# Optimization experiments

Measured on AMD Instinct MI355X. Metric: run time of the kernel, lower is better.

## Reference

```python
import jax, jax.numpy as jnp
import numpy as np

# Grid / model constants (from cfg: scene_bbox [0,0,0,102.4,102.4,6.4], featmap_size=quant_size=0.4, n_input=5, batch=2)
B, N = 2, 300000
X, Y, Z, T = 256, 256, 16, 5
QUANT = np.array([0.4, 0.4, 0.4, 1.0], dtype=np.float32)
C_MID, N_CLASSES = 8, 1  # MinkUNet14 INIT_DIM=8, out=n_classes=1
KOFF = 3  # 3^4 = 81 kernel offsets of the first 4D sparse conv


def setup_inputs() -> dict:
    key = jax.random.key(0)
    ks = jax.random.split(key, 5)
    xyz = jax.random.uniform(ks[0], (B, N, 3), dtype=jnp.float32) * jnp.array([102.4, 102.4, 6.4], jnp.float32)
    t = jax.random.randint(ks[1], (B, N, 1), 0, T).astype(jnp.float32)
    points = jnp.concatenate([xyz, t], axis=-1)  # [B, N, 4] 4D point clouds (x,y,z,t)
    W0 = jax.random.normal(ks[2], (KOFF**4, 1, C_MID), jnp.float32) * 0.1  # per-offset GEMM weights
    b0 = jnp.zeros((C_MID,), jnp.float32)
    W1 = jax.random.normal(ks[3], (C_MID, N_CLASSES), jnp.float32) * 0.1  # pointwise head
    b1 = jnp.zeros((N_CLASSES,), jnp.float32)
    return {"points": points, "W0": W0, "b0": b0, "W1": W1, "b1": b1}


def _voxelize(points):
    """Quantize 4D points and unweighted-average per-voxel features (ME.TensorField.sparse())."""
    coords = jnp.floor(points / jnp.asarray(QUANT)).astype(jnp.int32)  # [B, N, 4]
    cx = jnp.clip(coords[..., 0], 0, X - 1)
    cy = jnp.clip(coords[..., 1], 0, Y - 1)
    cz = jnp.clip(coords[..., 2], 0, Z - 1)
    ct = jnp.clip(coords[..., 3], 0, T - 1)
    lin = ((cx * Y + cy) * Z + cz) * T + ct            # [B, N] linear voxel index
    lin = (lin + jnp.arange(B, dtype=jnp.int32)[:, None] * (X * Y * Z * T)).reshape(-1)
    feats = jnp.full((B * N,), 0.5, points.dtype)      # feats = 0.5 * ones(len(pcd), 1)
    nseg = B * X * Y * Z * T
    s = jax.ops.segment_sum(feats, lin, num_segments=nseg)
    cnt = jax.ops.segment_sum(jnp.ones_like(feats), lin, num_segments=nseg)
    occ = cnt > 0
    avg = jnp.where(occ, s / jnp.maximum(cnt, 1.0), 0.0)
    grid = avg.reshape(B, X, Y, Z, T, 1)               # densified sparse features (zeros at empty voxels)
    mask = occ.reshape(B, X, Y, Z, T, 1).astype(points.dtype)
    return grid, mask


def reference(points, W0, b0, W1, b1):
    grid, mask = _voxelize(points)
    # 4D generalized sparse conv (kernel 3^4), stride 1: out coords == in coords.
    # Densified form: shift-gather neighbors, GEMM with per-offset weights, accumulate, mask to occupied voxels.
    pad = jnp.pad(grid, ((0, 0), (1, 1), (1, 1), (1, 1), (1, 1), (0, 0)))
    out = jnp.zeros(grid.shape[:-1] + (C_MID,), grid.dtype)
    k = 0
    for dx in range(KOFF):
        for dy in range(KOFF):
            for dz in range(KOFF):
                for dt in range(KOFF):
                    nb = pad[:, dx:dx + X, dy:dy + Y, dz:dz + Z, dt:dt + T, :]  # [B,X,Y,Z,T,1]
                    out = out + nb @ W0[k]
                    k += 1
    out = jax.nn.relu((out + b0) * mask)
    out = (out @ W1 + b1) * mask                        # pointwise sparse conv to n_classes
    return jnp.moveaxis(out, -1, 1)                     # dense featmap [B, 1, X, Y, Z, T]
```

## Files before the change

### kernel.cpp

```cpp
#include <hip/hip_runtime.h>

#define XD 256
#define YD 256
#define ZD 16
#define TD 5
#define BD 2
#define NP 300000
#define CMID 8
#define VPB (XD * YD * ZD * TD)
#define NVOX (BD * VPB)
#define MAXPTS (BD * NP)

#define OCC8_BYTES (BD * XD * YD * ZD * 8)
#define OCC8_U128  (OCC8_BYTES / 16)
#define NCOL   (BD * XD * YD)

#define SCAT_BLOCKS ((MAXPTS + 255) / 256)
#define CONV_BLOCKS 4096
#define CTHR 128
#define QCAP 512

__global__ __launch_bounds__(256) void zero_kernel(uint4* __restrict__ occ) {
    int i = blockIdx.x * 256 + threadIdx.x;
    uint4 z = {0u, 0u, 0u, 0u};
    for (int j = i; j < OCC8_U128; j += 2048 * 256) occ[j] = z;
}

__global__ __launch_bounds__(256) void scatter_kernel(
    const float4* __restrict__ pts, unsigned char* __restrict__ occ8) {
    int i = blockIdx.x * 256 + threadIdx.x;
    if (i >= MAXPTS) return;
    float4 p = pts[i];
    int cx = min(max((int)floorf(p.x / 0.4f), 0), XD - 1);
    int cy = min(max((int)floorf(p.y / 0.4f), 0), YD - 1);
    int cz = min(max((int)floorf(p.z / 0.4f), 0), ZD - 1);
    int ct = min(max((int)floorf(p.w / 1.0f), 0), TD - 1);
    int b  = i / NP;
    unsigned a = (((unsigned)b << 23) | ((unsigned)cx << 15) |
                  ((unsigned)cy << 7) | ((unsigned)cz << 3) | (unsigned)ct);
    occ8[a] = 1;
}

__device__ __forceinline__ unsigned pack8(unsigned long long v) {
    v |= v >> 7;
    v |= v >> 14;
    v |= v >> 28;
    return (unsigned)v & 0xffu;
}

__global__ __launch_bounds__(256) void pack_kernel(
    const ulonglong2* __restrict__ occ16, unsigned short* __restrict__ pk) {
    int j = blockIdx.x * 256 + threadIdx.x;
    ulonglong2 v = occ16[j];
    pk[j] = (unsigned short)(pack8(v.x) | (pack8(v.y) << 8));
}

__global__ __launch_bounds__(CTHR) void conv_kernel(
    const ulonglong2* __restrict__ pk128,
    const float* __restrict__ W0,
    const float* __restrict__ b0,
    const float* __restrict__ W1,
    const float* __restrict__ b1,
    float4* __restrict__ out4) {
    __shared__ float w0s[81 * 12];
    __shared__ unsigned long long clo[3 * 34];
    __shared__ unsigned long long chi[3 * 34];
    __shared__ unsigned short queue[QCAP];
    __shared__ float outt[32 * 80];
    __shared__ unsigned wsum[2];
    __shared__ float b0s[CMID];
    __shared__ float w1s[CMID];
    __shared__ float b1sv;

    int tid = threadIdx.x;
    int s   = blockIdx.x;
    int b   = s >> 11;
    int x   = (s >> 3) & 255;
    int ny0 = (s & 7) << 5;

    float4* ot4 = (float4*)outt;
    float4 zf = {0.f, 0.f, 0.f, 0.f};
#pragma unroll
    for (int j = 0; j < 5; ++j) ot4[tid + j * CTHR] = zf;

    if (tid < 81) {
#pragma unroll
        for (int c = 0; c < CMID; ++c) w0s[tid * 12 + c] = W0[tid * CMID + c];
    }
    if (tid < CMID) {
        b0s[tid] = b0[tid];
        w1s[tid] = W1[tid];
    }
    if (tid == 0) b1sv = b1[0];

    if (tid < 3 * 34) {
        int r   = tid / 34;
        int cyl = tid % 34;
        int nx  = x + r - 1;
        int cy  = ny0 + cyl - 1;
        bool valid = ((unsigned)nx < XD) && ((unsigned)cy < YD);
        ulonglong2 v = pk128[(b << 16) | ((nx & 255) << 8) | (cy & 255)];
        clo[tid] = valid ? v.x : 0ull;
        chi[tid] = valid ? v.y : 0ull;
    }
    __syncthreads();

    unsigned long long cw = (tid & 2) ? chi[35 + (tid >> 2)]
                                      : clo[35 + (tid >> 2)];
    unsigned w = (unsigned)((tid & 1) ? (cw >> 32) : cw);
    int cnt = __popc(w);

    unsigned pre = (unsigned)cnt;
#pragma unroll
    for (int off = 1; off < 64; off <<= 1) {
        unsigned v = (unsigned)__shfl_up((int)pre, off, 64);
        if ((tid & 63) >= off) pre += v;
    }
    int wv = tid >> 6;
    if ((tid & 63) == 63) wsum[wv] = pre;
    __syncthreads();
    unsigned qlen = wsum[0] + wsum[1];
    if (qlen > QCAP) qlen = QCAP;
    unsigned pos = ((wv == 1) ? wsum[0] : 0u) + pre - (unsigned)cnt;

    {
        int cl = tid >> 2;
        int zb = (tid & 3) << 2;
        unsigned ww = w;
        while (ww) {
            int bi = __ffs(ww) - 1;
            ww &= ww - 1;
            int zz = zb + (bi >> 3);
            int tt = bi & 7;
            if (pos < QCAP)
                queue[pos] = (unsigned short)((cl << 7) | (zz << 3) | tt);
            ++pos;
        }
    }
    __syncthreads();

    for (unsigned q = tid; q < qlen; q += CTHR) {
        int e  = queue[q];
        int cl = e >> 7;
        int z  = (e >> 3) & 15;
        int t  = e & 7;

        unsigned long long mpA = 0ull;
        unsigned mpB = 0u;
        int sft = (z - 1) * 8;
#pragma unroll
        for (int dxi = 0; dxi < 3; ++dxi) {
#pragma unroll
            for (int dyi = 0; dyi < 3; ++dyi) {
                int ci = dxi * 34 + cl + dyi;
                unsigned long long lo = clo[ci];
                unsigned long long hi = chi[ci];
                unsigned long long wv64 =
                    (z == 0) ? (lo << 8)
                  : (z <= 8) ? ((lo >> sft) | ((hi << 1) << (63 - sft)))
                             : (hi >> (sft - 64));
                unsigned qw = (((unsigned)wv64 & 0xffffffu) << 1) >> t;
                unsigned nine = (qw & 7u) | (((qw >> 8) & 7u) << 3) |
                                (((qw >> 16) & 7u) << 6);
                int c9 = dxi * 3 + dyi;
                if (c9 < 7) mpA |= (unsigned long long)nine << (9 * c9);
                else if (c9 == 7) mpB |= nine;
                else mpB |= nine << 9;
            }
        }

        float4 h0 = zf, h1 = zf;
        while (mpA) {
            int j = __ffsll((unsigned long long)mpA) - 1;
            mpA &= mpA - 1;
            const float4* row = (const float4*)&w0s[j * 12];
            h0 += row[0];
            h1 += row[1];
        }
        while (mpB) {
            int j = __ffs(mpB) - 1;
            mpB &= mpB - 1;
            const float4* row = (const float4*)&w0s[(63 + j) * 12];
            h0 += row[0];
            h1 += row[1];
        }

        float hc[CMID] = {h0.x, h0.y, h0.z, h0.w, h1.x, h1.y, h1.z, h1.w};
        float o = 0.0f;
#pragma unroll
        for (int c = 0; c < CMID; ++c) {
            float v = 0.5f * hc[c] + b0s[c];
            v = v > 0.0f ? v : 0.0f;
            o += v * w1s[c];
        }
        outt[cl * 80 + z * 5 + t] = o + b1sv;
    }
    __syncthreads();

    const float4* src = (const float4*)outt;
    float4* dst = out4 + ((size_t)b * (VPB / 4)) + (size_t)(x * YD + ny0) * 20;
#pragma unroll
    for (int j = 0; j < 5; ++j) dst[tid + j * CTHR] = src[tid + j * CTHR];
}

extern "C" void kernel_launch(void* const* d_in, const int* in_sizes, int n_in,
                              void* d_out, int out_size, void* d_ws, size_t ws_size,
                              hipStream_t stream) {
    const float4* pts = (const float4*)d_in[0];
    const float* W0   = (const float*)d_in[1];
    const float* b0   = (const float*)d_in[2];
    const float* W1   = (const float*)d_in[3];
    const float* b1   = (const float*)d_in[4];
    unsigned char* occ8 = (unsigned char*)d_ws;
    unsigned short* pk  = (unsigned short*)((char*)d_ws + OCC8_BYTES);

    zero_kernel<<<2048, 256, 0, stream>>>((uint4*)occ8);
    scatter_kernel<<<SCAT_BLOCKS, 256, 0, stream>>>(pts, occ8);
    pack_kernel<<<OCC8_U128 / 256, 256, 0, stream>>>(
        (const ulonglong2*)occ8, pk);
    conv_kernel<<<CONV_BLOCKS, 128, 0, stream>>>(
        (const ulonglong2*)pk, W0, b0, W1, b1, (float4*)d_out);
}
```

Before: 42.88 us.

## Process two points per thread in scatter and two voxels per thread in conv

```diff
diff --git a/kernel.cpp b/kernel.cpp
--- a/kernel.cpp
+++ b/kernel.cpp
@@ -15,7 +15,7 @@
 #define OCC8_U128  (OCC8_BYTES / 16)
 #define NCOL   (BD * XD * YD)
 
-#define SCAT_BLOCKS ((MAXPTS + 255) / 256)
+#define SCAT_BLOCKS ((MAXPTS / 2 + 255) / 256)
 #define CONV_BLOCKS 4096
 #define CTHR 128
 #define QCAP 512
@@ -28,17 +28,21 @@
 
 __global__ __launch_bounds__(256) void scatter_kernel(
     const float4* __restrict__ pts, unsigned char* __restrict__ occ8) {
-    int i = blockIdx.x * 256 + threadIdx.x;
-    if (i >= MAXPTS) return;
-    float4 p = pts[i];
-    int cx = min(max((int)floorf(p.x / 0.4f), 0), XD - 1);
-    int cy = min(max((int)floorf(p.y / 0.4f), 0), YD - 1);
-    int cz = min(max((int)floorf(p.z / 0.4f), 0), ZD - 1);
-    int ct = min(max((int)floorf(p.w / 1.0f), 0), TD - 1);
-    int b  = i / NP;
-    unsigned a = (((unsigned)b << 23) | ((unsigned)cx << 15) |
-                  ((unsigned)cy << 7) | ((unsigned)cz << 3) | (unsigned)ct);
-    occ8[a] = 1;
+    int i = (blockIdx.x * 256 + threadIdx.x) * 2;
+#pragma unroll
+    for (int k = 0; k < 2; ++k) {
+        int idx = i + k;
+        if (idx >= MAXPTS) break;
+        float4 p = pts[idx];
+        int cx = min(max((int)floorf(p.x / 0.4f), 0), XD - 1);
+        int cy = min(max((int)floorf(p.y / 0.4f), 0), YD - 1);
+        int cz = min(max((int)floorf(p.z / 0.4f), 0), ZD - 1);
+        int ct = min(max((int)floorf(p.w / 1.0f), 0), TD - 1);
+        int b  = idx / NP;
+        unsigned a = (((unsigned)b << 23) | ((unsigned)cx << 15) |
+                      ((unsigned)cy << 7) | ((unsigned)cz << 3) | (unsigned)ct);
+        __builtin_nontemporal_store((unsigned char)1, &occ8[a]);
+    }
 }
 
 __device__ __forceinline__ unsigned pack8(unsigned long long v) {
@@ -53,6 +57,34 @@
     int j = blockIdx.x * 256 + threadIdx.x;
     ulonglong2 v = occ16[j];
     pk[j] = (unsigned short)(pack8(v.x) | (pack8(v.y) << 8));
+}
+
+__device__ __forceinline__ void build_mask81(
+    const unsigned long long* clo, const unsigned long long* chi,
+    int cl, int z, int t, unsigned long long& mpA, unsigned& mpB) {
+    mpA = 0ull;
+    mpB = 0u;
+    int sft = (z - 1) * 8;
+#pragma unroll
+    for (int dxi = 0; dxi < 3; ++dxi) {
+#pragma unroll
+        for (int dyi = 0; dyi < 3; ++dyi) {
+            int ci = dxi * 34 + cl + dyi;
+            unsigned long long lo = clo[ci];
+            unsigned long long hi = chi[ci];
+            unsigned long long wv64 =
+                (z == 0) ? (lo << 8)
+              : (z <= 8) ? ((lo >> sft) | ((hi << 1) << (63 - sft)))
+                         : (hi >> (sft - 64));
+            unsigned qw = (((unsigned)wv64 & 0xffffffu) << 1) >> t;
+            unsigned nine = (qw & 7u) | (((qw >> 8) & 7u) << 3) |
+                            (((qw >> 16) & 7u) << 6);
+            int c9 = dxi * 3 + dyi;
+            if (c9 < 7) mpA |= (unsigned long long)nine << (9 * c9);
+            else if (c9 == 7) mpB |= nine;
+            else mpB |= nine << 9;
+        }
+    }
 }
 
 __global__ __launch_bounds__(CTHR) void conv_kernel(
@@ -84,8 +116,9 @@
     for (int j = 0; j < 5; ++j) ot4[tid + j * CTHR] = zf;
 
     if (tid < 81) {
-#pragma unroll
-        for (int c = 0; c < CMID; ++c) w0s[tid * 12 + c] = W0[tid * CMID + c];
+        const float4* src = (const float4*)(W0 + tid * CMID);
+        *(float4*)&w0s[tid * 12]     = src[0];
+        *(float4*)&w0s[tid * 12 + 4] = src[1];
     }
     if (tid < CMID) {
         b0s[tid] = b0[tid];
@@ -139,61 +172,66 @@
     }
     __syncthreads();
 
-    for (unsigned q = tid; q < qlen; q += CTHR) {
-        int e  = queue[q];
-        int cl = e >> 7;
-        int z  = (e >> 3) & 15;
-        int t  = e & 7;
-
-        unsigned long long mpA = 0ull;
-        unsigned mpB = 0u;
-        int sft = (z - 1) * 8;
-#pragma unroll
-        for (int dxi = 0; dxi < 3; ++dxi) {
-#pragma unroll
-            for (int dyi = 0; dyi < 3; ++dyi) {
-                int ci = dxi * 34 + cl + dyi;
-                unsigned long long lo = clo[ci];
-                unsigned long long hi = chi[ci];
-                unsigned long long wv64 =
-                    (z == 0) ? (lo << 8)
-                  : (z <= 8) ? ((lo >> sft) | ((hi << 1) << (63 - sft)))
-                             : (hi >> (sft - 64));
-                unsigned qw = (((unsigned)wv64 & 0xffffffu) << 1) >> t;
-                unsigned nine = (qw & 7u) | (((qw >> 8) & 7u) << 3) |
-                                (((qw >> 16) & 7u) << 6);
-                int c9 = dxi * 3 + dyi;
-                if (c9 < 7) mpA |= (unsigned long long)nine << (9 * c9);
-                else if (c9 == 7) mpB |= nine;
-                else mpB |= nine << 9;
-            }
-        }
-
-        float4 h0 = zf, h1 = zf;
-        while (mpA) {
-            int j = __ffsll((unsigned long long)mpA) - 1;
-            mpA &= mpA - 1;
+    for (unsigned base = 0; base < qlen; base += 2 * CTHR) {
+        unsigned q0 = base + 2 * (unsigned)tid;
+        if (q0 >= qlen) continue;
+        unsigned q1 = q0 + 1;
+        bool v1 = (q1 < qlen);
+
+        int e0 = queue[q0];
+        int e1 = queue[v1 ? q1 : q0];
+        int cl0 = e0 >> 7, z0 = (e0 >> 3) & 15, t0 = e0 & 7;
+        int cl1 = e1 >> 7, z1 = (e1 >> 3) & 15, t1 = e1 & 7;
+
+        unsigned long long mpA0, mpA1;
+        unsigned mpB0, mpB1;
+        build_mask81(clo, chi, cl0, z0, t0, mpA0, mpB0);
+        build_mask81(clo, chi, cl1, z1, t1, mpA1, mpB1);
+
+        float4 h0 = zf, h1 = zf, g0 = zf, g1 = zf;
+        while (mpA0) {
+            int j = __ffsll(mpA0) - 1;
+            mpA0 &= mpA0 - 1;
             const float4* row = (const float4*)&w0s[j * 12];
             h0 += row[0];
             h1 += row[1];
         }
-        while (mpB) {
-            int j = __ffs(mpB) - 1;
-            mpB &= mpB - 1;
+        while (mpB0) {
+            int j = __ffs(mpB0) - 1;
+            mpB0 &= mpB0 - 1;
             const float4* row = (const float4*)&w0s[(63 + j) * 12];
             h0 += row[0];
             h1 += row[1];
         }
-
-        float hc[CMID] = {h0.x, h0.y, h0.z, h0.w, h1.x, h1.y, h1.z, h1.w};
-        float o = 0.0f;
+        while (mpA1) {
+            int j = __ffsll(mpA1) - 1;
+            mpA1 &= mpA1 - 1;
+            const float4* row = (const float4*)&w0s[j * 12];
+            g0 += row[0];
+            g1 += row[1];
+        }
+        while (mpB1) {
+            int j = __ffs(mpB1) - 1;
+            mpB1 &= mpB1 - 1;
+            const float4* row = (const float4*)&w0s[(63 + j) * 12];
+            g0 += row[0];
+            g1 += row[1];
+        }
+
+        float hc0[CMID] = {h0.x, h0.y, h0.z, h0.w, h1.x, h1.y, h1.z, h1.w};
+        float hc1[CMID] = {g0.x, g0.y, g0.z, g0.w, g1.x, g1.y, g1.z, g1.w};
+        float o0 = 0.0f, o1 = 0.0f;
 #pragma unroll
         for (int c = 0; c < CMID; ++c) {
-            float v = 0.5f * hc[c] + b0s[c];
-            v = v > 0.0f ? v : 0.0f;
-            o += v * w1s[c];
-        }
-        outt[cl * 80 + z * 5 + t] = o + b1sv;
+            float a = 0.5f * hc0[c] + b0s[c];
+            a = a > 0.0f ? a : 0.0f;
+            o0 += a * w1s[c];
+            float d = 0.5f * hc1[c] + b0s[c];
+            d = d > 0.0f ? d : 0.0f;
+            o1 += d * w1s[c];
+        }
+        outt[cl0 * 80 + z0 * 5 + t0] = o0 + b1sv;
+        if (v1) outt[cl1 * 80 + z1 * 5 + t1] = o1 + b1sv;
     }
     __syncthreads();
 
```

After: 53.18 us. 24.0% more time.
